# Kernel optimization log

Hardware: AMD Instinct MI355X
Metric: run time of the kernel (lower is better)

## Reference

```python
import jax, jax.numpy as jnp
import numpy as np

ALPHA = 0.2  # LeakyReLU negative slope
NEG_INF = -9e15


def setup_inputs() -> dict:
    key = jax.random.key(0)
    k1, k2, k3, k4 = jax.random.split(key, 4)
    B, N, F_in, F_out = 8, 2048, 256, 128
    x = jax.random.normal(k1, (B, N, F_in), dtype=jnp.float32)
    adj = jax.random.randint(k2, (B, N, N), 0, 2, dtype=jnp.int32)
    # xavier-uniform-like init
    limW = float(np.sqrt(6.0 / (F_in + F_out)))
    W = jax.random.uniform(k3, (F_in, F_out), jnp.float32, -limW, limW)
    lima = float(np.sqrt(6.0 / (2 * F_out + 1)))
    a = jax.random.uniform(k4, (2 * F_out, 1), jnp.float32, -lima, lima)
    return {"x": x, "adj": adj, "W": W, "a": a}


def reference(x, adj, W, a):
    # x: [B, N, F_in], adj: [B, N, N], W: [F_in, F_out], a: [2*F_out, 1]
    F_out = W.shape[1]
    h = jnp.einsum('bnf,fo->bno', x, W)            # [B, N, F_out]
    a1 = a[:F_out, 0]                               # attends to source node i
    a2 = a[F_out:, 0]                               # attends to target node j
    f1 = h @ a1                                     # [B, N]
    f2 = h @ a2                                     # [B, N]
    # e[b,i,j] = leakyrelu(a1.h_i + a2.h_j) -- factored form of the concat trick
    e = jax.nn.leaky_relu(f1[:, :, None] + f2[:, None, :], negative_slope=ALPHA)
    attention = jnp.where(adj > 0, e, NEG_INF)
    attention = jax.nn.softmax(attention, axis=2)   # [B, N, N]
    # dropout is identity in eval mode
    h_prime = jnp.einsum('bij,bjo->bio', attention, h)  # [B, N, F_out]
    return jax.nn.elu(h_prime)                      # concat=True -> ELU
```

## Files before the change

### kernel.cpp

```cpp
#include <hip/hip_runtime.h>
#include <stdint.h>

#define BB   8
#define NN   2048
#define FIN  256
#define FOUT 128

using short8 = __attribute__((ext_vector_type(8))) short;
using f32x4  = __attribute__((ext_vector_type(4))) float;

__device__ __forceinline__ unsigned short rbf(float f) {
    return (unsigned short)((__float_as_uint(f) + 0x8000u) >> 16);
}

__device__ __forceinline__ void mfma_calib(int m, int quad, int* Mlab, int* Nlab) {
    short8 pa1, pb1, pa2, pb2;
    const short one = (short)0x3F80;
    const short mb  = (short)rbf((float)m);
#pragma unroll
    for (int j = 0; j < 8; ++j) { pa1[j] = 0; pa2[j] = 0; pb1[j] = mb; pb2[j] = one; }
    if (quad == 0) { pa1[0] = one; pa2[0] = mb; }
    f32x4 zz = {0.f, 0.f, 0.f, 0.f};
    f32x4 c1 = __builtin_amdgcn_mfma_f32_16x16x32_bf16(pa1, pb1, zz, 0, 0, 0);
    f32x4 c2 = __builtin_amdgcn_mfma_f32_16x16x32_bf16(pa2, pb2, zz, 0, 0, 0);
#pragma unroll
    for (int r = 0; r < 4; ++r) {
        Nlab[r] = ((int)c1[r]) & 15;
        Mlab[r] = ((int)c2[r]) & 15;
    }
}

__global__ __launch_bounds__(256) void gat_wt(const float* __restrict__ W,
                                              unsigned short* __restrict__ wt) {
    const int g  = blockIdx.x * 256 + threadIdx.x;
    const int k  = g >> 5;
    const int o4 = (g & 31) << 2;
    float4 wv = *(const float4*)(W + (k << 7) + o4);
    wt[((o4 + 0) << 8) + k] = rbf(wv.x);
    wt[((o4 + 1) << 8) + k] = rbf(wv.y);
    wt[((o4 + 2) << 8) + k] = rbf(wv.z);
    wt[((o4 + 3) << 8) + k] = rbf(wv.w);
}

__global__ __launch_bounds__(256) void gat_h3(
        const float* __restrict__ x, const unsigned short* __restrict__ wt,
        const float* __restrict__ a, unsigned short* __restrict__ ht,
        float* __restrict__ f1, float* __restrict__ f2) {
    __shared__ unsigned short xs[16][264];
    __shared__ float hs[16][132];
    const int bk   = blockIdx.x;
    const int R0   = bk << 4;
    const int b    = R0 >> 11;
    const int il0  = R0 & (NN - 1);
    const int tid  = threadIdx.x;
    const int w    = tid >> 6;
    const int lane = tid & 63;
    const int m    = lane & 15;
    const int quad = lane >> 4;

#pragma unroll
    for (int rr = 0; rr < 4; ++rr) {
        const int row = (w << 2) + rr;
        float4 xv = *(const float4*)(x + (size_t)(R0 + row) * FIN + (lane << 2));
        ushort4 c4;
        c4.x = rbf(xv.x); c4.y = rbf(xv.y); c4.z = rbf(xv.z); c4.w = rbf(xv.w);
        *(ushort4*)(&xs[row][lane << 2]) = c4;
    }
    int Mlab[4], Nlab[4];
    mfma_calib(m, quad, Mlab, Nlab);
    __syncthreads();

    f32x4 zz = {0.f, 0.f, 0.f, 0.f};
    f32x4 acc[2] = {zz, zz};
#pragma unroll
    for (int kc = 0; kc < 8; ++kc) {
        const int k0 = (kc << 5) + (quad << 3);
        short8 av = *(const short8*)(&xs[m][k0]);
#pragma unroll
        for (int t = 0; t < 2; ++t) {
            const int ot = (w << 1) + t;
            short8 bw = *(const short8*)(wt + (((ot << 4) + m) << 8) + k0);
            acc[t] = __builtin_amdgcn_mfma_f32_16x16x32_bf16(av, bw, acc[t], 0, 0, 0);
        }
    }
#pragma unroll
    for (int t = 0; t < 2; ++t)
#pragma unroll
        for (int r = 0; r < 4; ++r)
            hs[Mlab[r]][(((w << 1) + t) << 4) + Nlab[r]] = acc[t][r];
    __syncthreads();

    {
        const int i   = tid >> 4;
        const int seg = tid & 15;
        const int o0  = seg << 3;
        float s1 = 0.f, s2 = 0.f;
#pragma unroll
        for (int e = 0; e < 8; ++e) {
            float hv = hs[i][o0 + e];
            s1 = fmaf(hv, a[o0 + e], s1);
            s2 = fmaf(hv, a[FOUT + o0 + e], s2);
        }
        s1 += __shfl_xor(s1, 1); s1 += __shfl_xor(s1, 2);
        s1 += __shfl_xor(s1, 4); s1 += __shfl_xor(s1, 8);
        s2 += __shfl_xor(s2, 1); s2 += __shfl_xor(s2, 2);
        s2 += __shfl_xor(s2, 4); s2 += __shfl_xor(s2, 8);
        if (seg == 0) { f1[R0 + i] = s1; f2[R0 + i] = s2; }
    }
    {
        const int o  = tid >> 1;
        const int i8 = (tid & 1) << 3;
        short8 hv;
#pragma unroll
        for (int e = 0; e < 8; ++e) hv[e] = (short)rbf(hs[i8 + e][o]);
        *(short8*)(ht + ((size_t)((b << 7) + o) << 11) + il0 + i8) = hv;
    }
}

__global__ __launch_bounds__(256, 2) void gat_s4(
        const int* __restrict__ adj, const unsigned short* __restrict__ ht,
        const float* __restrict__ f1, const float* __restrict__ f2,
        float* __restrict__ out) {
    const int bk   = blockIdx.x;
    const int b    = bk & 7;
    const int i0   = (bk >> 3) << 5;
    const int tid  = threadIdx.x;
    const int w    = tid >> 6;
    const int lane = tid & 63;
    const int m    = lane & 15;
    const int quad = lane >> 4;

    __shared__ float accb[2][32][128];
    __shared__ float sbuf[4][2][16];

    int Mlab[4], Nlab[4];
    mfma_calib(m, quad, Mlab, Nlab);

    const int gi0 = (b << 11) + i0;
    const float f1a = f1[gi0 + m];
    const float f1b = f1[gi0 + 16 + m];
    const int* adjr0 = adj + ((size_t)(gi0 + m) << 11);
    const int* adjr1 = adj + ((size_t)(gi0 + 16 + m) << 11);
    const float* f2b = f2 + (b << 11);
    const unsigned short* htb = ht + ((size_t)b << 18);

    f32x4 zz = {0.f, 0.f, 0.f, 0.f};
    f32x4 acc1[8], acc2[8];
#pragma unroll
    for (int t = 0; t < 8; ++t) { acc1[t] = zz; acc2[t] = zz; }
    float s1 = 0.f, s2 = 0.f;

    const int jb = (w << 9) + (quad << 3);
#pragma unroll 2
    for (int c = 0; c < 16; ++c) {
        const int j0 = jb + (c << 5);
        short8 hf[8];
#pragma unroll
        for (int ot = 0; ot < 8; ++ot)
            hf[ot] = *(const short8*)(htb + ((size_t)((ot << 4) + m) << 11) + j0);

        int4   aA0 = *(const int4*)(adjr0 + j0);
        int4   aA1 = *(const int4*)(adjr0 + j0 + 4);
        int4   aB0 = *(const int4*)(adjr1 + j0);
        int4   aB1 = *(const int4*)(adjr1 + j0 + 4);
        float4 fa  = *(const float4*)(f2b + j0);
        float4 fb  = *(const float4*)(f2b + j0 + 4);
        float fm[8] = {fa.x, fa.y, fa.z, fa.w, fb.x, fb.y, fb.z, fb.w};

        float pA[8], pB[8];
        {
            int am[8] = {aA0.x, aA0.y, aA0.z, aA0.w, aA1.x, aA1.y, aA1.z, aA1.w};
#pragma unroll
            for (int u = 0; u < 8; ++u) {
                float e = f1a + fm[u];
                pA[u] = (am[u] > 0) ? __expf(fmaxf(e, 0.2f * e)) : 0.f;
            }
        }
        {
            int bm[8] = {aB0.x, aB0.y, aB0.z, aB0.w, aB1.x, aB1.y, aB1.z, aB1.w};
#pragma unroll
            for (int u = 0; u < 8; ++u) {
                float e = f1b + fm[u];
                pB[u] = (bm[u] > 0) ? __expf(fmaxf(e, 0.2f * e)) : 0.f;
            }
        }
        s1 += ((pA[0] + pA[1]) + (pA[2] + pA[3])) + ((pA[4] + pA[5]) + (pA[6] + pA[7]));
        s2 += ((pB[0] + pB[1]) + (pB[2] + pB[3])) + ((pB[4] + pB[5]) + (pB[6] + pB[7]));

        short8 pf1, pf2;
#pragma unroll
        for (int u = 0; u < 8; ++u) { pf1[u] = (short)rbf(pA[u]); pf2[u] = (short)rbf(pB[u]); }

#pragma unroll
        for (int ot = 0; ot < 8; ++ot) {
            acc1[ot] = __builtin_amdgcn_mfma_f32_16x16x32_bf16(pf1, hf[ot], acc1[ot], 0, 0, 0);
            acc2[ot] = __builtin_amdgcn_mfma_f32_16x16x32_bf16(pf2, hf[ot], acc2[ot], 0, 0, 0);
        }
    }

    s1 += __shfl_xor(s1, 16); s1 += __shfl_xor(s1, 32);
    s2 += __shfl_xor(s2, 16); s2 += __shfl_xor(s2, 32);
    if (lane < 16) { sbuf[w][0][lane] = s1; sbuf[w][1][lane] = s2; }

    if (w < 2) {
#pragma unroll
        for (int ot = 0; ot < 8; ++ot)
#pragma unroll
            for (int r = 0; r < 4; ++r) {
                accb[w][Mlab[r]][(ot << 4) + Nlab[r]]      = acc1[ot][r];
                accb[w][16 + Mlab[r]][(ot << 4) + Nlab[r]] = acc2[ot][r];
            }
    }
    __syncthreads();
    if (w >= 2) {
#pragma unroll
        for (int ot = 0; ot < 8; ++ot)
#pragma unroll
            for (int r = 0; r < 4; ++r) {
                accb[w - 2][Mlab[r]][(ot << 4) + Nlab[r]]      += acc1[ot][r];
                accb[w - 2][16 + Mlab[r]][(ot << 4) + Nlab[r]] += acc2[ot][r];
            }
    }
    __syncthreads();

    {
        const int row = tid >> 3;
        const int o0  = (tid & 7) << 4;
        const int g   = row >> 4;
        const int mm  = row & 15;
        const float s = (sbuf[0][g][mm] + sbuf[1][g][mm]) +
                        (sbuf[2][g][mm] + sbuf[3][g][mm]);
        const float inv = 1.0f / s;
        float* orow = out + (((size_t)gi0 + row) << 7) + o0;
#pragma unroll
        for (int v4 = 0; v4 < 4; ++v4) {
            float4 rv;
            float y;
            y = (accb[0][row][o0 + 4 * v4 + 0] + accb[1][row][o0 + 4 * v4 + 0]) * inv;
            rv.x = y > 0.f ? y : expm1f(y);
            y = (accb[0][row][o0 + 4 * v4 + 1] + accb[1][row][o0 + 4 * v4 + 1]) * inv;
            rv.y = y > 0.f ? y : expm1f(y);
            y = (accb[0][row][o0 + 4 * v4 + 2] + accb[1][row][o0 + 4 * v4 + 2]) * inv;
            rv.z = y > 0.f ? y : expm1f(y);
            y = (accb[0][row][o0 + 4 * v4 + 3] + accb[1][row][o0 + 4 * v4 + 3]) * inv;
            rv.w = y > 0.f ? y : expm1f(y);
            *(float4*)(orow + 4 * v4) = rv;
        }
    }
}

extern "C" void kernel_launch(void* const* d_in, const int* in_sizes, int n_in,
                              void* d_out, int out_size, void* d_ws, size_t ws_size,
                              hipStream_t stream) {
    const float* x   = nullptr;
    const int*   adj = nullptr;
    const float* W   = nullptr;
    const float* a   = nullptr;
    for (int i = 0; i < n_in; ++i) {
        const long s = in_sizes[i];
        if      (s == (long)BB * NN * NN)  adj = (const int*)d_in[i];
        else if (s == (long)BB * NN * FIN) x   = (const float*)d_in[i];
        else if (s == (long)FIN * FOUT)    W   = (const float*)d_in[i];
        else if (s == 2L * FOUT)           a   = (const float*)d_in[i];
    }
    if (!x)   x   = (const float*)d_in[0];
    if (!adj) adj = (const int*)d_in[1];
    if (!W)   W   = (const float*)d_in[2];
    if (!a)   a   = (const float*)d_in[3];
    float* out = (float*)d_out;

    unsigned short* wt = (unsigned short*)d_ws;
    unsigned short* ht = wt + 32768;
    float* f1 = (float*)(ht + (size_t)BB * NN * FOUT);
    float* f2 = f1 + BB * NN;

    hipLaunchKernelGGL(gat_wt, dim3(32),   dim3(256), 0, stream, W, wt);
    hipLaunchKernelGGL(gat_h3, dim3(1024), dim3(256), 0, stream, x, wt, a, ht, f1, f2);
    hipLaunchKernelGGL(gat_s4, dim3(512),  dim3(256), 0, stream, adj, ht, f1, f2, out);
}
```

Measured before the change: 247.1 us.

## Precompute adjacency bitmask and software-pipeline the attention-aggregation loop

Adds a separate kernel that packs the int32 adjacency matrix into a one-bit-per-entry mask, so the main aggregation kernel reads bytes instead of int4 vectors. The main loop is restructured into a two-stage double-buffered load/compute pipeline, which hides the global load latency for ht, the mask and f2. The calibration MFMA is moved after the loop. The full 128MB adjacency is still read once by the new pack kernel, so the total adj traffic is unchanged, and the pipeline adds register pressure under the 2-blocks-per-CU launch bound.

```diff
diff --git a/kernel.cpp b/kernel.cpp
--- a/kernel.cpp
+++ b/kernel.cpp
@@ -40,6 +40,24 @@
     wt[((o4 + 1) << 8) + k] = rbf(wv.y);
     wt[((o4 + 2) << 8) + k] = rbf(wv.z);
     wt[((o4 + 3) << 8) + k] = rbf(wv.w);
+}
+
+__global__ __launch_bounds__(256) void gat_bm(const int* __restrict__ adj,
+                                              unsigned char* __restrict__ bm) {
+    const int row = blockIdx.x;
+    const int tid = threadIdx.x;
+    const int4* p = (const int4*)(adj + ((size_t)row << 11) + (tid << 3));
+    int4 a0 = p[0];
+    int4 a1 = p[1];
+    unsigned int b = (unsigned int)(a0.x > 0)
+                   | ((unsigned int)(a0.y > 0) << 1)
+                   | ((unsigned int)(a0.z > 0) << 2)
+                   | ((unsigned int)(a0.w > 0) << 3)
+                   | ((unsigned int)(a1.x > 0) << 4)
+                   | ((unsigned int)(a1.y > 0) << 5)
+                   | ((unsigned int)(a1.z > 0) << 6)
+                   | ((unsigned int)(a1.w > 0) << 7);
+    bm[(row << 8) + tid] = (unsigned char)b;
 }
 
 __global__ __launch_bounds__(256) void gat_h3(
@@ -117,8 +135,44 @@
     }
 }
 
-__global__ __launch_bounds__(256, 2) void gat_s4(
-        const int* __restrict__ adj, const unsigned short* __restrict__ ht,
+#define LOADC(H, MskA, MskB, Fa, Fb, c) { \
+    const int j0_ = jb + ((c) << 5); \
+    _Pragma("unroll") \
+    for (int ot = 0; ot < 8; ++ot) \
+        H[ot] = *(const short8*)(htb + ((size_t)((ot << 4) + m) << 11) + j0_); \
+    MskA = bmr0[mbb + ((c) << 2)]; \
+    MskB = bmr1[mbb + ((c) << 2)]; \
+    Fa = *(const float4*)(f2b + j0_); \
+    Fb = *(const float4*)(f2b + j0_ + 4); \
+}
+
+#define COMPC(H, MskA, MskB, Fa, Fb) { \
+    float fm_[8] = {Fa.x, Fa.y, Fa.z, Fa.w, Fb.x, Fb.y, Fb.z, Fb.w}; \
+    float pA_[8], pB_[8]; \
+    _Pragma("unroll") \
+    for (int u = 0; u < 8; ++u) { \
+        float e = f1a + fm_[u]; \
+        pA_[u] = (MskA & (1u << u)) ? __expf(fmaxf(e, 0.2f * e)) : 0.f; \
+    } \
+    _Pragma("unroll") \
+    for (int u = 0; u < 8; ++u) { \
+        float e = f1b + fm_[u]; \
+        pB_[u] = (MskB & (1u << u)) ? __expf(fmaxf(e, 0.2f * e)) : 0.f; \
+    } \
+    s1 += ((pA_[0]+pA_[1])+(pA_[2]+pA_[3]))+((pA_[4]+pA_[5])+(pA_[6]+pA_[7])); \
+    s2 += ((pB_[0]+pB_[1])+(pB_[2]+pB_[3]))+((pB_[4]+pB_[5])+(pB_[6]+pB_[7])); \
+    short8 pf1_, pf2_; \
+    _Pragma("unroll") \
+    for (int u = 0; u < 8; ++u) { pf1_[u] = (short)rbf(pA_[u]); pf2_[u] = (short)rbf(pB_[u]); } \
+    _Pragma("unroll") \
+    for (int ot = 0; ot < 8; ++ot) { \
+        acc1[ot] = __builtin_amdgcn_mfma_f32_16x16x32_bf16(pf1_, H[ot], acc1[ot], 0, 0, 0); \
+        acc2[ot] = __builtin_amdgcn_mfma_f32_16x16x32_bf16(pf2_, H[ot], acc2[ot], 0, 0, 0); \
+    } \
+}
+
+__global__ __launch_bounds__(256, 2) void gat_s5(
+        const unsigned char* __restrict__ bm, const unsigned short* __restrict__ ht,
         const float* __restrict__ f1, const float* __restrict__ f2,
         float* __restrict__ out) {
     const int bk   = blockIdx.x;
@@ -133,74 +187,45 @@
     __shared__ float accb[2][32][128];
     __shared__ float sbuf[4][2][16];
 
-    int Mlab[4], Nlab[4];
-    mfma_calib(m, quad, Mlab, Nlab);
-
     const int gi0 = (b << 11) + i0;
     const float f1a = f1[gi0 + m];
     const float f1b = f1[gi0 + 16 + m];
-    const int* adjr0 = adj + ((size_t)(gi0 + m) << 11);
-    const int* adjr1 = adj + ((size_t)(gi0 + 16 + m) << 11);
+    const unsigned char* bmr0 = bm + ((size_t)(gi0 + m) << 8);
+    const unsigned char* bmr1 = bm + ((size_t)(gi0 + 16 + m) << 8);
     const float* f2b = f2 + (b << 11);
     const unsigned short* htb = ht + ((size_t)b << 18);
 
+    const int jb  = (w << 9) + (quad << 3);
+    const int mbb = (w << 6) + quad;
+
     f32x4 zz = {0.f, 0.f, 0.f, 0.f};
     f32x4 acc1[8], acc2[8];
 #pragma unroll
     for (int t = 0; t < 8; ++t) { acc1[t] = zz; acc2[t] = zz; }
     float s1 = 0.f, s2 = 0.f;
 
-    const int jb = (w << 9) + (quad << 3);
-#pragma unroll 2
-    for (int c = 0; c < 16; ++c) {
-        const int j0 = jb + (c << 5);
-        short8 hf[8];
-#pragma unroll
-        for (int ot = 0; ot < 8; ++ot)
-            hf[ot] = *(const short8*)(htb + ((size_t)((ot << 4) + m) << 11) + j0);
-
-        int4   aA0 = *(const int4*)(adjr0 + j0);
-        int4   aA1 = *(const int4*)(adjr0 + j0 + 4);
-        int4   aB0 = *(const int4*)(adjr1 + j0);
-        int4   aB1 = *(const int4*)(adjr1 + j0 + 4);
-        float4 fa  = *(const float4*)(f2b + j0);
-        float4 fb  = *(const float4*)(f2b + j0 + 4);
-        float fm[8] = {fa.x, fa.y, fa.z, fa.w, fb.x, fb.y, fb.z, fb.w};
-
-        float pA[8], pB[8];
-        {
-            int am[8] = {aA0.x, aA0.y, aA0.z, aA0.w, aA1.x, aA1.y, aA1.z, aA1.w};
-#pragma unroll
-            for (int u = 0; u < 8; ++u) {
-                float e = f1a + fm[u];
-                pA[u] = (am[u] > 0) ? __expf(fmaxf(e, 0.2f * e)) : 0.f;
-            }
-        }
-        {
-            int bm[8] = {aB0.x, aB0.y, aB0.z, aB0.w, aB1.x, aB1.y, aB1.z, aB1.w};
-#pragma unroll
-            for (int u = 0; u < 8; ++u) {
-                float e = f1b + fm[u];
-                pB[u] = (bm[u] > 0) ? __expf(fmaxf(e, 0.2f * e)) : 0.f;
-            }
-        }
-        s1 += ((pA[0] + pA[1]) + (pA[2] + pA[3])) + ((pA[4] + pA[5]) + (pA[6] + pA[7]));
-        s2 += ((pB[0] + pB[1]) + (pB[2] + pB[3])) + ((pB[4] + pB[5]) + (pB[6] + pB[7]));
-
-        short8 pf1, pf2;
-#pragma unroll
-        for (int u = 0; u < 8; ++u) { pf1[u] = (short)rbf(pA[u]); pf2[u] = (short)rbf(pB[u]); }
-
-#pragma unroll
-        for (int ot = 0; ot < 8; ++ot) {
-            acc1[ot] = __builtin_amdgcn_mfma_f32_16x16x32_bf16(pf1, hf[ot], acc1[ot], 0, 0, 0);
-            acc2[ot] = __builtin_amdgcn_mfma_f32_16x16x32_bf16(pf2, hf[ot], acc2[ot], 0, 0, 0);
-        }
-    }
+    short8 hfA[8], hfB[8];
+    unsigned int mA0, mB0, mA1, mB1;
+    float4 faA, fbA, faB, fbB;
+
+    LOADC(hfA, mA0, mB0, faA, fbA, 0);
+    for (int cc = 0; cc < 7; ++cc) {
+        const int c0 = cc << 1;
+        LOADC(hfB, mA1, mB1, faB, fbB, c0 + 1);
+        COMPC(hfA, mA0, mB0, faA, fbA);
+        LOADC(hfA, mA0, mB0, faA, fbA, c0 + 2);
+        COMPC(hfB, mA1, mB1, faB, fbB);
+    }
+    LOADC(hfB, mA1, mB1, faB, fbB, 15);
+    COMPC(hfA, mA0, mB0, faA, fbA);
+    COMPC(hfB, mA1, mB1, faB, fbB);
 
     s1 += __shfl_xor(s1, 16); s1 += __shfl_xor(s1, 32);
     s2 += __shfl_xor(s2, 16); s2 += __shfl_xor(s2, 32);
     if (lane < 16) { sbuf[w][0][lane] = s1; sbuf[w][1][lane] = s2; }
+
+    int Mlab[4], Nlab[4];
+    mfma_calib(m, quad, Mlab, Nlab);
 
     if (w < 2) {
 #pragma unroll
@@ -271,10 +296,12 @@
 
     unsigned short* wt = (unsigned short*)d_ws;
     unsigned short* ht = wt + 32768;
-    float* f1 = (float*)(ht + (size_t)BB * NN * FOUT);
-    float* f2 = f1 + BB * NN;
-
-    hipLaunchKernelGGL(gat_wt, dim3(32),   dim3(256), 0, stream, W, wt);
-    hipLaunchKernelGGL(gat_h3, dim3(1024), dim3(256), 0, stream, x, wt, a, ht, f1, f2);
-    hipLaunchKernelGGL(gat_s4, dim3(512),  dim3(256), 0, stream, adj, ht, f1, f2, out);
-}
+    float* f1  = (float*)(ht + (size_t)BB * NN * FOUT);
+    float* f2  = f1 + BB * NN;
+    unsigned char* bmw = (unsigned char*)(f2 + BB * NN);
+
+    hipLaunchKernelGGL(gat_wt,  dim3(32),    dim3(256), 0, stream, W, wt);
+    hipLaunchKernelGGL(gat_bm,  dim3(16384), dim3(256), 0, stream, adj, bmw);
+    hipLaunchKernelGGL(gat_h3,  dim3(1024),  dim3(256), 0, stream, x, wt, a, ht, f1, f2);
+    hipLaunchKernelGGL(gat_s5,  dim3(512),   dim3(256), 0, stream, bmw, ht, f1, f2, out);
+}
```

Result: slower. 261.6 us (+5.9%).
